# Optimization experiments

Hardware: AMD Instinct MI355X
Metric: run time of the kernel (lower is better)

The kernel has to match this reference:

```python
import jax, jax.numpy as jnp
import numpy as np

N = 10000        # num nodes
E = 640000       # num edges
FIN = 128        # input feature dim
NH = 8           # num heads
FOUT = 16        # out features per head (NH*FOUT == FIN)
NEG_SLOPE = 0.2
EPS = 1e-16


def setup_inputs() -> dict:
    key = jax.random.key(0)
    ks = jax.random.split(key, 7)
    x = jax.random.normal(ks[0], (N, FIN), dtype=jnp.float32)
    edges = jax.random.randint(ks[1], (2, E), 0, N, dtype=jnp.int64)
    # kaiming-uniform-ish init scale
    s = float(np.sqrt(6.0 / FIN))
    W_proj = jax.random.uniform(ks[2], (NH * FOUT, FIN), minval=-s, maxval=s, dtype=jnp.float32)
    W_skip = jax.random.uniform(ks[3], (NH * FOUT, FIN), minval=-s, maxval=s, dtype=jnp.float32)
    sf = float(np.sqrt(6.0 / FOUT))
    score_src = jax.random.uniform(ks[4], (1, NH, FOUT), minval=-sf, maxval=sf, dtype=jnp.float32)
    score_tgt = jax.random.uniform(ks[5], (1, NH, FOUT), minval=-sf, maxval=sf, dtype=jnp.float32)
    bias = jnp.zeros((NH * FOUT,), dtype=jnp.float32)
    return {"x": x, "edges": edges, "W_proj": W_proj, "W_skip": W_skip,
            "score_src": score_src, "score_tgt": score_tgt, "bias": bias}


def reference(x, edges, W_proj, W_skip, score_src, score_tgt, bias):
    src, tgt = edges[0], edges[1]
    # project: [N, NH, FOUT]
    proj = (x @ W_proj.T).reshape(N, NH, FOUT)
    # per-node scores: [N, NH]
    s_src = (proj * score_src).sum(-1)
    s_tgt = (proj * score_tgt).sum(-1)
    # lift to edges and score: [E, NH]
    scores = jax.nn.leaky_relu(s_src[src] + s_tgt[tgt], negative_slope=NEG_SLOPE)
    # neighborhood-aware softmax (global max subtraction, as in original)
    exp_scores = jnp.exp(scores - jnp.max(scores))
    denom = jax.ops.segment_sum(exp_scores, tgt, num_segments=N)  # [N, NH]
    att = exp_scores / (denom[tgt] + EPS)                          # [E, NH]
    # weighted aggregation: [N, NH, FOUT]
    weighted = proj[src] * att[:, :, None]
    out = jax.ops.segment_sum(weighted, tgt, num_segments=N)
    # skip connection (dims differ per-head, so skip_proj is used), concat, bias
    out = out + (x @ W_skip.T).reshape(N, NH, FOUT)
    out = out.reshape(N, NH * FOUT) + bias
    return out
```

## Files before the change

### kernel.cpp

```cpp
#include <hip/hip_runtime.h>
#include <hip/hip_bf16.h>

#define FIN   128
#define NH    8
#define NEG   0.2f
#define HB    128
#define NMAX  10240

typedef __attribute__((ext_vector_type(8))) short short8;
typedef __attribute__((ext_vector_type(4))) float f32x4;

__device__ __forceinline__ short f2bf(float f) {
    unsigned u = __float_as_uint(f);
    return (short)((u + 0x7FFFu + ((u >> 16) & 1u)) >> 16);
}
__device__ __forceinline__ float bflo(unsigned p) { return __uint_as_float(p << 16); }
__device__ __forceinline__ float bfhi(unsigned p) { return __uint_as_float(p & 0xFFFF0000u); }
__device__ __forceinline__ float ld_f(const void* p, int i, bool bf16) {
    if (bf16) {
        unsigned h = ((const unsigned short*)p)[i];
        return __uint_as_float(h << 16);
    }
    return ((const float*)p)[i];
}
__device__ __forceinline__ short8 ld_frag(const void* p, size_t off, bool bf16) {
    if (bf16) return *(const short8*)((const short*)p + off);
    const float* f = (const float*)p + off;
    f32x4 f0 = *(const f32x4*)f;
    f32x4 f1 = *(const f32x4*)(f + 4);
    short8 r;
    r[0] = f2bf(f0[0]); r[1] = f2bf(f0[1]); r[2] = f2bf(f0[2]); r[3] = f2bf(f0[3]);
    r[4] = f2bf(f1[0]); r[5] = f2bf(f1[1]); r[6] = f2bf(f1[2]); r[7] = f2bf(f1[3]);
    return r;
}
__device__ __forceinline__ float escore(float ss, float st) {
    float v = ss + st;
    v = v > 0.f ? v : NEG * v;
    return __expf(fminf(v, 60.f));
}
__device__ __forceinline__ bool wave_bf16(const unsigned* x32) {
    unsigned w  = x32[threadIdx.x & 63];
    unsigned ex = (w >> 7) & 0xFFu;
    return __popcll(__ballot(ex >= 118u && ex <= 130u)) >= 48;
}
__device__ __forceinline__ bool wave_e64(const int* e32) {
    return __popcll(__ballot(e32[2 * (threadIdx.x & 63) + 1] == 0)) == 64;
}

__global__ __launch_bounds__(256) void k_projhist(
    const void* __restrict__ x, const void* __restrict__ Wp,
    const void* __restrict__ Ws,
    const void* __restrict__ ssrcw, const void* __restrict__ stgtw,
    unsigned short* __restrict__ projb, unsigned short* __restrict__ skipb,
    float* __restrict__ s_src, float* __restrict__ s_tgt,
    const int* __restrict__ e32, int* __restrict__ hist2d,
    int N, int E, int tiles, int halfTiles, int projBlocks, int perB)
{
    __shared__ unsigned l32[NMAX / 2];
    if ((int)blockIdx.x >= projBlocks) {
        const bool e64 = wave_e64(e32);
        const int hb = (int)blockIdx.x - projBlocks;
        const int t = threadIdx.x;
        const int nw = (N + 1) >> 1;
        for (int j = t; j < nw; j += 256) l32[j] = 0;
        __syncthreads();
        const int lo = hb * perB;
        const int hi = min(lo + perB, E);
        for (int i = lo + t; i < hi; i += 256) {
            int tg = e64 ? e32[2 * ((size_t)E + i)] : e32[(size_t)E + i];
            atomicAdd(&l32[tg >> 1], 1u << ((tg & 1) << 4));
        }
        __syncthreads();
        for (int j = t; j < N; j += 256)
            hist2d[(size_t)hb * N + j] = (l32[j >> 1] >> ((j & 1) << 4)) & 0xFFFFu;
        return;
    }
    const bool bf16 = wave_bf16((const unsigned*)x);
    const int lane = threadIdx.x & 63;
    const int wt = blockIdx.x * 4 + (threadIdx.x >> 6);
    if (wt >= tiles) return;
    const int mat = (wt >= halfTiles) ? 1 : 0;
    const int m0 = (mat ? wt - halfTiles : wt) * 16;
    const int mr = lane & 15;
    const int kb = lane >> 4;

    short8 a[4];
    const size_t xoff = (size_t)(m0 + mr) * FIN + kb * 8;
#pragma unroll
    for (int s = 0; s < 4; ++s) a[s] = ld_frag(x, xoff + s * 32, bf16);

    const void* W = mat ? Ws : Wp;
    f32x4 acc[8];
#pragma unroll
    for (int c = 0; c < 8; ++c) {
        acc[c] = (f32x4){0.f, 0.f, 0.f, 0.f};
        const size_t woff = (size_t)(c * 16 + mr) * FIN + kb * 8;
#pragma unroll
        for (int s = 0; s < 4; ++s) {
            short8 b = ld_frag(W, woff + s * 32, bf16);
            acc[c] = __builtin_amdgcn_mfma_f32_16x16x32_bf16(a[s], b, acc[c], 0, 0, 0);
        }
    }
    if (mat == 0) {
#pragma unroll
        for (int c = 0; c < 8; ++c) {
            float sw = ld_f(ssrcw, c * 16 + mr, bf16);
            float tw = ld_f(stgtw, c * 16 + mr, bf16);
#pragma unroll
            for (int r = 0; r < 4; ++r) {
                int row = m0 + kb * 4 + r;
                float v = acc[c][r];
                projb[(size_t)row * FIN + c * 16 + mr] = (unsigned short)f2bf(v);
                float vs = v * sw, vt = v * tw;
#pragma unroll
                for (int o = 8; o >= 1; o >>= 1) {
                    vs += __shfl_xor(vs, o);
                    vt += __shfl_xor(vt, o);
                }
                if (mr == 0) {
                    s_src[row * NH + c] = vs;
                    s_tgt[row * NH + c] = vt;
                }
            }
        }
    } else {
#pragma unroll
        for (int c = 0; c < 8; ++c)
#pragma unroll
            for (int r = 0; r < 4; ++r)
                skipb[(size_t)(m0 + kb * 4 + r) * FIN + c * 16 + mr] =
                    (unsigned short)f2bf(acc[c][r]);
    }
}

__global__ __launch_bounds__(256) void k_colscan(
    const int* __restrict__ hist2d, int* __restrict__ pbase,
    int* __restrict__ cnt, int N)
{
    int j = blockIdx.x * 256 + threadIdx.x;
    if (j >= N) return;
    int s = 0;
#pragma unroll 4
    for (int b = 0; b < HB; ++b) {
        int v = hist2d[(size_t)b * N + j];
        pbase[(size_t)b * N + j] = s;
        s += v;
    }
    cnt[j] = s;
}

__global__ __launch_bounds__(256) void k_offscan(const int* __restrict__ cnt,
                                                 int* __restrict__ offs, int N)
{
    const int t = threadIdx.x;
    const int PER = (N + 255) / 256;
    const int base = t * PER;
    int local[40];
    int sum = 0;
    for (int i = 0; i < PER && i < 40; ++i) {
        int idx = base + i;
        int v = (idx < N) ? cnt[idx] : 0;
        local[i] = sum;
        sum += v;
    }
    __shared__ int sd[256];
    sd[t] = sum;
    __syncthreads();
#pragma unroll
    for (int off = 1; off < 256; off <<= 1) {
        int add = (t >= off) ? sd[t - off] : 0;
        __syncthreads();
        sd[t] += add;
        __syncthreads();
    }
    int excl = sd[t] - sum;
    for (int i = 0; i < PER && i < 40; ++i) {
        int idx = base + i;
        if (idx < N) offs[idx] = excl + local[i];
    }
    if (t == 255) offs[N] = sd[255];
}

__global__ __launch_bounds__(256) void k_place(
    const int* __restrict__ e32, const int* __restrict__ offs,
    const int* __restrict__ pbase, int* __restrict__ sorted_src,
    int N, int E, int perB)
{
    __shared__ int cur[NMAX];
    const bool e64 = wave_e64(e32);
    const int b = blockIdx.x, t = threadIdx.x;
    for (int j = t; j < N; j += 256)
        cur[j] = offs[j] + pbase[(size_t)b * N + j];
    __syncthreads();
    const int lo = b * perB;
    const int hi = min(lo + perB, E);
    for (int i = lo + t; i < hi; i += 256) {
        int s, tg;
        if (e64) { s = e32[2 * (size_t)i]; tg = e32[2 * ((size_t)E + i)]; }
        else     { s = e32[i];             tg = e32[(size_t)E + i]; }
        int pos = atomicAdd(&cur[tg], 1);
        sorted_src[pos] = s;
    }
}

__global__ __launch_bounds__(64) void k_aggregate(
    const int* __restrict__ offs, const int* __restrict__ sorted_src,
    const float* __restrict__ s_src, const float* __restrict__ s_tgt,
    const unsigned short* __restrict__ projb, const unsigned short* __restrict__ skipb,
    const void* __restrict__ bias, void* __restrict__ out,
    const unsigned* __restrict__ x32)
{
    const bool bf16 = wave_bf16(x32);
    const int n = blockIdx.x, l = threadIdx.x;
    const int start = offs[n], end = offs[n + 1];
    const int h = l >> 3;
    const int c2 = l * 2;
    const float st = s_tgt[(size_t)n * NH + h];

    float ae0 = 0.f, ao0 = 0.f, ae1 = 0.f, ao1 = 0.f;
    float ae2 = 0.f, ao2 = 0.f, ae3 = 0.f, ao3 = 0.f;
    float d0 = 0.f, d1 = 0.f, d2 = 0.f, d3 = 0.f;
    int e = start;
    for (; e + 4 <= end; e += 4) {
        int s0 = sorted_src[e],     s1 = sorted_src[e + 1];
        int s2 = sorted_src[e + 2], s3 = sorted_src[e + 3];
        float w0 = escore(s_src[(size_t)s0 * NH + h], st);
        float w1 = escore(s_src[(size_t)s1 * NH + h], st);
        float w2 = escore(s_src[(size_t)s2 * NH + h], st);
        float w3 = escore(s_src[(size_t)s3 * NH + h], st);
        unsigned p0 = *(const unsigned*)(projb + (size_t)s0 * FIN + c2);
        unsigned p1 = *(const unsigned*)(projb + (size_t)s1 * FIN + c2);
        unsigned p2 = *(const unsigned*)(projb + (size_t)s2 * FIN + c2);
        unsigned p3 = *(const unsigned*)(projb + (size_t)s3 * FIN + c2);
        ae0 += w0 * bflo(p0); ao0 += w0 * bfhi(p0); d0 += w0;
        ae1 += w1 * bflo(p1); ao1 += w1 * bfhi(p1); d1 += w1;
        ae2 += w2 * bflo(p2); ao2 += w2 * bfhi(p2); d2 += w2;
        ae3 += w3 * bflo(p3); ao3 += w3 * bfhi(p3); d3 += w3;
    }
    for (; e < end; ++e) {
        int s = sorted_src[e];
        float w = escore(s_src[(size_t)s * NH + h], st);
        unsigned p = *(const unsigned*)(projb + (size_t)s * FIN + c2);
        ae0 += w * bflo(p); ao0 += w * bfhi(p); d0 += w;
    }

    float inv = 1.f / (((d0 + d1) + (d2 + d3)) + 1e-16f);
    unsigned skp = *(const unsigned*)(skipb + (size_t)n * FIN + c2);
    float be, bo;
    if (bf16) {
        unsigned bb = *(const unsigned*)((const unsigned short*)bias + c2);
        be = bflo(bb); bo = bfhi(bb);
    } else {
        float2 b2 = *(const float2*)((const float*)bias + c2);
        be = b2.x; bo = b2.y;
    }
    float oe = ((ae0 + ae1) + (ae2 + ae3)) * inv + bflo(skp) + be;
    float oo = ((ao0 + ao1) + (ao2 + ao3)) * inv + bfhi(skp) + bo;
    if (bf16) {
        unsigned pr = ((unsigned)(unsigned short)f2bf(oo) << 16)
                    | (unsigned)(unsigned short)f2bf(oe);
        ((unsigned*)out)[((size_t)n * FIN + c2) >> 1] = pr;
    } else {
        float2 o2; o2.x = oe; o2.y = oo;
        *(float2*)((float*)out + (size_t)n * FIN + c2) = o2;
    }
}

extern "C" void kernel_launch(void* const* d_in, const int* in_sizes, int n_in,
                              void* d_out, int out_size, void* d_ws, size_t ws_size,
                              hipStream_t stream)
{
    const void* x    = d_in[0];
    const int* edges = (const int*)d_in[1];
    const void* Wp   = d_in[2];
    const void* Ws   = d_in[3];
    const void* ssw  = d_in[4];
    const void* stw  = d_in[5];
    const void* bias = d_in[6];

    const int N = in_sizes[0] / FIN;
    const int E = in_sizes[1] / 2;

    unsigned short* projb = (unsigned short*)d_ws;
    unsigned short* skipb = projb + (size_t)N * FIN;
    float* s_src    = (float*)(skipb + (size_t)N * FIN);
    float* s_tgt    = s_src + (size_t)N * NH;
    int* sorted_src = (int*)(s_tgt + (size_t)N * NH);
    int* offs       = sorted_src + E;
    int* cnt        = offs + (N + 1);
    int* hist2d     = cnt + N;
    int* pbase      = hist2d + (size_t)HB * N;

    const int halfTiles  = (N + 15) / 16;
    const int tiles      = 2 * halfTiles;
    const int projBlocks = (tiles + 3) / 4;
    const int perB       = (E + HB - 1) / HB;

    k_projhist<<<projBlocks + HB, 256, 0, stream>>>(
        x, Wp, Ws, ssw, stw, projb, skipb, s_src, s_tgt,
        edges, hist2d, N, E, tiles, halfTiles, projBlocks, perB);
    k_colscan<<<(N + 255) / 256, 256, 0, stream>>>(hist2d, pbase, cnt, N);
    k_offscan<<<1, 256, 0, stream>>>(cnt, offs, N);
    k_place<<<HB, 256, 0, stream>>>(edges, offs, pbase, sorted_src, N, E, perB);
    k_aggregate<<<N, 64, 0, stream>>>(offs, sorted_src, s_src, s_tgt, projb,
                                      skipb, bias, d_out, (const unsigned*)x);
}
```

Measured before the change: 165.9 us.

## Fuse GAT pipeline into one cooperative persistent kernel with grid syncs

Replaces the five separate launches (projection+histogram, column scan, offset scan, placement, aggregation) with a single cooperative kernel of 960 blocks that separates phases with grid.sync. The offset scan becomes a two-level block scan spread over multiple blocks, and aggregation becomes a persistent wave loop over nodes. The aim is to remove launch gaps and the single-block offset scan, at the cost of grid-wide barriers, 40KB shared memory per block limiting occupancy, and less parallelism in the aggregation phase. If the cooperative launch fails, it falls back to the original multi-kernel path.

```diff
diff --git a/kernel.cpp b/kernel.cpp
--- a/kernel.cpp
+++ b/kernel.cpp
@@ -1,11 +1,17 @@
 #include <hip/hip_runtime.h>
 #include <hip/hip_bf16.h>
+#include <hip/hip_cooperative_groups.h>
+
+namespace cg = cooperative_groups;
 
 #define FIN   128
 #define NH    8
 #define NEG   0.2f
 #define HB    128
 #define NMAX  10240
+#define GW0   512
+#define GRID  960
+#define TPB   256
 
 typedef __attribute__((ext_vector_type(8))) short short8;
 typedef __attribute__((ext_vector_type(4))) float f32x4;
@@ -47,38 +53,13 @@
     return __popcll(__ballot(e32[2 * (threadIdx.x & 63) + 1] == 0)) == 64;
 }
 
-__global__ __launch_bounds__(256) void k_projhist(
-    const void* __restrict__ x, const void* __restrict__ Wp,
-    const void* __restrict__ Ws,
-    const void* __restrict__ ssrcw, const void* __restrict__ stgtw,
-    unsigned short* __restrict__ projb, unsigned short* __restrict__ skipb,
-    float* __restrict__ s_src, float* __restrict__ s_tgt,
-    const int* __restrict__ e32, int* __restrict__ hist2d,
-    int N, int E, int tiles, int halfTiles, int projBlocks, int perB)
-{
-    __shared__ unsigned l32[NMAX / 2];
-    if ((int)blockIdx.x >= projBlocks) {
-        const bool e64 = wave_e64(e32);
-        const int hb = (int)blockIdx.x - projBlocks;
-        const int t = threadIdx.x;
-        const int nw = (N + 1) >> 1;
-        for (int j = t; j < nw; j += 256) l32[j] = 0;
-        __syncthreads();
-        const int lo = hb * perB;
-        const int hi = min(lo + perB, E);
-        for (int i = lo + t; i < hi; i += 256) {
-            int tg = e64 ? e32[2 * ((size_t)E + i)] : e32[(size_t)E + i];
-            atomicAdd(&l32[tg >> 1], 1u << ((tg & 1) << 4));
-        }
-        __syncthreads();
-        for (int j = t; j < N; j += 256)
-            hist2d[(size_t)hb * N + j] = (l32[j >> 1] >> ((j & 1) << 4)) & 0xFFFFu;
-        return;
-    }
+__device__ __forceinline__ void gemm_tile(
+    int wt, int halfTiles, const void* x, const void* Wp, const void* Ws,
+    const void* ssrcw, const void* stgtw,
+    unsigned short* projb, unsigned short* skipb, float* s_src, float* s_tgt)
+{
     const bool bf16 = wave_bf16((const unsigned*)x);
     const int lane = threadIdx.x & 63;
-    const int wt = blockIdx.x * 4 + (threadIdx.x >> 6);
-    if (wt >= tiles) return;
     const int mat = (wt >= halfTiles) ? 1 : 0;
     const int m0 = (mat ? wt - halfTiles : wt) * 16;
     const int mr = lane & 15;
@@ -133,85 +114,13 @@
     }
 }
 
-__global__ __launch_bounds__(256) void k_colscan(
-    const int* __restrict__ hist2d, int* __restrict__ pbase,
-    int* __restrict__ cnt, int N)
-{
-    int j = blockIdx.x * 256 + threadIdx.x;
-    if (j >= N) return;
-    int s = 0;
-#pragma unroll 4
-    for (int b = 0; b < HB; ++b) {
-        int v = hist2d[(size_t)b * N + j];
-        pbase[(size_t)b * N + j] = s;
-        s += v;
-    }
-    cnt[j] = s;
-}
-
-__global__ __launch_bounds__(256) void k_offscan(const int* __restrict__ cnt,
-                                                 int* __restrict__ offs, int N)
-{
-    const int t = threadIdx.x;
-    const int PER = (N + 255) / 256;
-    const int base = t * PER;
-    int local[40];
-    int sum = 0;
-    for (int i = 0; i < PER && i < 40; ++i) {
-        int idx = base + i;
-        int v = (idx < N) ? cnt[idx] : 0;
-        local[i] = sum;
-        sum += v;
-    }
-    __shared__ int sd[256];
-    sd[t] = sum;
-    __syncthreads();
-#pragma unroll
-    for (int off = 1; off < 256; off <<= 1) {
-        int add = (t >= off) ? sd[t - off] : 0;
-        __syncthreads();
-        sd[t] += add;
-        __syncthreads();
-    }
-    int excl = sd[t] - sum;
-    for (int i = 0; i < PER && i < 40; ++i) {
-        int idx = base + i;
-        if (idx < N) offs[idx] = excl + local[i];
-    }
-    if (t == 255) offs[N] = sd[255];
-}
-
-__global__ __launch_bounds__(256) void k_place(
-    const int* __restrict__ e32, const int* __restrict__ offs,
-    const int* __restrict__ pbase, int* __restrict__ sorted_src,
-    int N, int E, int perB)
-{
-    __shared__ int cur[NMAX];
-    const bool e64 = wave_e64(e32);
-    const int b = blockIdx.x, t = threadIdx.x;
-    for (int j = t; j < N; j += 256)
-        cur[j] = offs[j] + pbase[(size_t)b * N + j];
-    __syncthreads();
-    const int lo = b * perB;
-    const int hi = min(lo + perB, E);
-    for (int i = lo + t; i < hi; i += 256) {
-        int s, tg;
-        if (e64) { s = e32[2 * (size_t)i]; tg = e32[2 * ((size_t)E + i)]; }
-        else     { s = e32[i];             tg = e32[(size_t)E + i]; }
-        int pos = atomicAdd(&cur[tg], 1);
-        sorted_src[pos] = s;
-    }
-}
-
-__global__ __launch_bounds__(64) void k_aggregate(
-    const int* __restrict__ offs, const int* __restrict__ sorted_src,
-    const float* __restrict__ s_src, const float* __restrict__ s_tgt,
-    const unsigned short* __restrict__ projb, const unsigned short* __restrict__ skipb,
-    const void* __restrict__ bias, void* __restrict__ out,
-    const unsigned* __restrict__ x32)
-{
-    const bool bf16 = wave_bf16(x32);
-    const int n = blockIdx.x, l = threadIdx.x;
+__device__ __forceinline__ void agg_node(
+    int n, bool bf16, const int* offs, const int* sorted_src,
+    const float* s_src, const float* s_tgt,
+    const unsigned short* projb, const unsigned short* skipb,
+    const void* bias, void* out)
+{
+    const int l = threadIdx.x & 63;
     const int start = offs[n], end = offs[n + 1];
     const int h = l >> 3;
     const int c2 = l * 2;
@@ -266,6 +175,220 @@
     }
 }
 
+__global__ __launch_bounds__(TPB, 4) void k_gat(
+    const void* __restrict__ x, const void* __restrict__ Wp,
+    const void* __restrict__ Ws, const void* __restrict__ ssrcw,
+    const void* __restrict__ stgtw, const void* __restrict__ bias,
+    const int* __restrict__ e32, void* __restrict__ out,
+    unsigned short* __restrict__ projb, unsigned short* __restrict__ skipb,
+    float* __restrict__ s_src, float* __restrict__ s_tgt,
+    int* __restrict__ sorted_src, int* __restrict__ offs,
+    int* __restrict__ tmp_off, int* __restrict__ bt,
+    int* __restrict__ hist2d, int* __restrict__ pbase,
+    int N, int E, int perB, int tiles, int halfTiles)
+{
+    cg::grid_group grid = cg::this_grid();
+    __shared__ int sh[NMAX];
+    const int b = blockIdx.x, t = threadIdx.x;
+    const int wv = b * 4 + (t >> 6);
+
+    if (b < HB) {
+        const bool e64 = wave_e64(e32);
+        unsigned* l32 = (unsigned*)sh;
+        const int nw = (N + 1) >> 1;
+        for (int j = t; j < nw; j += TPB) l32[j] = 0;
+        __syncthreads();
+        const int lo = b * perB, hi = min(lo + perB, E);
+        for (int i = lo + t; i < hi; i += TPB) {
+            int tg = e64 ? e32[2 * ((size_t)E + i)] : e32[(size_t)E + i];
+            atomicAdd(&l32[tg >> 1], 1u << ((tg & 1) << 4));
+        }
+        __syncthreads();
+        for (int j = t; j < N; j += TPB)
+            hist2d[(size_t)b * N + j] = (l32[j >> 1] >> ((j & 1) << 4)) & 0xFFFFu;
+    } else {
+        const int wt = wv - GW0;
+        if (wt >= 0 && wt < tiles)
+            gemm_tile(wt, halfTiles, x, Wp, Ws, ssrcw, stgtw,
+                      projb, skipb, s_src, s_tgt);
+    }
+    grid.sync();
+
+    const int CB = (N + TPB - 1) / TPB;
+    if (b < CB) {
+        const int j = b * TPB + t;
+        int s = 0;
+        if (j < N) {
+            for (int r = 0; r < HB; ++r) {
+                int v = hist2d[(size_t)r * N + j];
+                pbase[(size_t)r * N + j] = s;
+                s += v;
+            }
+        }
+        sh[t] = s;
+        __syncthreads();
+#pragma unroll
+        for (int off = 1; off < TPB; off <<= 1) {
+            int add = (t >= off) ? sh[t - off] : 0;
+            __syncthreads();
+            sh[t] += add;
+            __syncthreads();
+        }
+        int incl = sh[t];
+        if (j < N) tmp_off[j] = incl - s;
+        if (t == TPB - 1) bt[b] = incl;
+    }
+    grid.sync();
+
+    if (b < CB) {
+        int carry = 0;
+        for (int r = 0; r < b; ++r) carry += bt[r];
+        const int j = b * TPB + t;
+        if (j < N) offs[j] = tmp_off[j] + carry;
+        if (b == CB - 1 && t == 0) offs[N] = carry + bt[b];
+    }
+    grid.sync();
+
+    if (b < HB) {
+        const bool e64 = wave_e64(e32);
+        for (int j = t; j < N; j += TPB)
+            sh[j] = offs[j] + pbase[(size_t)b * N + j];
+        __syncthreads();
+        const int lo = b * perB, hi = min(lo + perB, E);
+        for (int i = lo + t; i < hi; i += TPB) {
+            int s, tg;
+            if (e64) { s = e32[2 * (size_t)i]; tg = e32[2 * ((size_t)E + i)]; }
+            else     { s = e32[i];             tg = e32[(size_t)E + i]; }
+            int pos = atomicAdd(&sh[tg], 1);
+            sorted_src[pos] = s;
+        }
+    }
+    grid.sync();
+
+    {
+        const bool bf16 = wave_bf16((const unsigned*)x);
+        const int TOTW = (int)gridDim.x * 4;
+        for (int n = wv; n < N; n += TOTW)
+            agg_node(n, bf16, offs, sorted_src, s_src, s_tgt,
+                     projb, skipb, bias, out);
+    }
+}
+
+__global__ __launch_bounds__(256) void k_projhist(
+    const void* __restrict__ x, const void* __restrict__ Wp,
+    const void* __restrict__ Ws,
+    const void* __restrict__ ssrcw, const void* __restrict__ stgtw,
+    unsigned short* __restrict__ projb, unsigned short* __restrict__ skipb,
+    float* __restrict__ s_src, float* __restrict__ s_tgt,
+    const int* __restrict__ e32, int* __restrict__ hist2d,
+    int N, int E, int tiles, int halfTiles, int projBlocks, int perB)
+{
+    __shared__ unsigned l32[NMAX / 2];
+    if ((int)blockIdx.x >= projBlocks) {
+        const bool e64 = wave_e64(e32);
+        const int hb = (int)blockIdx.x - projBlocks;
+        const int t = threadIdx.x;
+        const int nw = (N + 1) >> 1;
+        for (int j = t; j < nw; j += 256) l32[j] = 0;
+        __syncthreads();
+        const int lo = hb * perB;
+        const int hi = min(lo + perB, E);
+        for (int i = lo + t; i < hi; i += 256) {
+            int tg = e64 ? e32[2 * ((size_t)E + i)] : e32[(size_t)E + i];
+            atomicAdd(&l32[tg >> 1], 1u << ((tg & 1) << 4));
+        }
+        __syncthreads();
+        for (int j = t; j < N; j += 256)
+            hist2d[(size_t)hb * N + j] = (l32[j >> 1] >> ((j & 1) << 4)) & 0xFFFFu;
+        return;
+    }
+    const int wt = blockIdx.x * 4 + (threadIdx.x >> 6);
+    if (wt >= tiles) return;
+    gemm_tile(wt, halfTiles, x, Wp, Ws, ssrcw, stgtw, projb, skipb, s_src, s_tgt);
+}
+
+__global__ __launch_bounds__(256) void k_colscan(
+    const int* __restrict__ hist2d, int* __restrict__ pbase,
+    int* __restrict__ cnt, int N)
+{
+    int j = blockIdx.x * 256 + threadIdx.x;
+    if (j >= N) return;
+    int s = 0;
+#pragma unroll 4
+    for (int b = 0; b < HB; ++b) {
+        int v = hist2d[(size_t)b * N + j];
+        pbase[(size_t)b * N + j] = s;
+        s += v;
+    }
+    cnt[j] = s;
+}
+
+__global__ __launch_bounds__(256) void k_offscan(const int* __restrict__ cnt,
+                                                 int* __restrict__ offs, int N)
+{
+    const int t = threadIdx.x;
+    const int PER = (N + 255) / 256;
+    const int base = t * PER;
+    int local[40];
+    int sum = 0;
+    for (int i = 0; i < PER && i < 40; ++i) {
+        int idx = base + i;
+        int v = (idx < N) ? cnt[idx] : 0;
+        local[i] = sum;
+        sum += v;
+    }
+    __shared__ int sd[256];
+    sd[t] = sum;
+    __syncthreads();
+#pragma unroll
+    for (int off = 1; off < 256; off <<= 1) {
+        int add = (t >= off) ? sd[t - off] : 0;
+        __syncthreads();
+        sd[t] += add;
+        __syncthreads();
+    }
+    int excl = sd[t] - sum;
+    for (int i = 0; i < PER && i < 40; ++i) {
+        int idx = base + i;
+        if (idx < N) offs[idx] = excl + local[i];
+    }
+    if (t == 255) offs[N] = sd[255];
+}
+
+__global__ __launch_bounds__(256) void k_place(
+    const int* __restrict__ e32, const int* __restrict__ offs,
+    const int* __restrict__ pbase, int* __restrict__ sorted_src,
+    int N, int E, int perB)
+{
+    __shared__ int cur[NMAX];
+    const bool e64 = wave_e64(e32);
+    const int b = blockIdx.x, t = threadIdx.x;
+    for (int j = t; j < N; j += 256)
+        cur[j] = offs[j] + pbase[(size_t)b * N + j];
+    __syncthreads();
+    const int lo = b * perB;
+    const int hi = min(lo + perB, E);
+    for (int i = lo + t; i < hi; i += 256) {
+        int s, tg;
+        if (e64) { s = e32[2 * (size_t)i]; tg = e32[2 * ((size_t)E + i)]; }
+        else     { s = e32[i];             tg = e32[(size_t)E + i]; }
+        int pos = atomicAdd(&cur[tg], 1);
+        sorted_src[pos] = s;
+    }
+}
+
+__global__ __launch_bounds__(64) void k_aggregate(
+    const int* __restrict__ offs, const int* __restrict__ sorted_src,
+    const float* __restrict__ s_src, const float* __restrict__ s_tgt,
+    const unsigned short* __restrict__ projb, const unsigned short* __restrict__ skipb,
+    const void* __restrict__ bias, void* __restrict__ out,
+    const unsigned* __restrict__ x32)
+{
+    const bool bf16 = wave_bf16(x32);
+    agg_node(blockIdx.x, bf16, offs, sorted_src, s_src, s_tgt,
+             projb, skipb, bias, out);
+}
+
 extern "C" void kernel_launch(void* const* d_in, const int* in_sizes, int n_in,
                               void* d_out, int out_size, void* d_ws, size_t ws_size,
                               hipStream_t stream)
@@ -277,9 +400,10 @@
     const void* ssw  = d_in[4];
     const void* stw  = d_in[5];
     const void* bias = d_in[6];
-
-    const int N = in_sizes[0] / FIN;
-    const int E = in_sizes[1] / 2;
+    void* out        = d_out;
+
+    int N = in_sizes[0] / FIN;
+    int E = in_sizes[1] / 2;
 
     unsigned short* projb = (unsigned short*)d_ws;
     unsigned short* skipb = projb + (size_t)N * FIN;
@@ -287,21 +411,35 @@
     float* s_tgt    = s_src + (size_t)N * NH;
     int* sorted_src = (int*)(s_tgt + (size_t)N * NH);
     int* offs       = sorted_src + E;
-    int* cnt        = offs + (N + 1);
+    int* tmp_off    = offs + (N + 1);
+    int* bt         = tmp_off + N;
+    int* cnt        = bt + 64;
     int* hist2d     = cnt + N;
     int* pbase      = hist2d + (size_t)HB * N;
 
-    const int halfTiles  = (N + 15) / 16;
-    const int tiles      = 2 * halfTiles;
-    const int projBlocks = (tiles + 3) / 4;
-    const int perB       = (E + HB - 1) / HB;
-
-    k_projhist<<<projBlocks + HB, 256, 0, stream>>>(
-        x, Wp, Ws, ssw, stw, projb, skipb, s_src, s_tgt,
-        edges, hist2d, N, E, tiles, halfTiles, projBlocks, perB);
-    k_colscan<<<(N + 255) / 256, 256, 0, stream>>>(hist2d, pbase, cnt, N);
-    k_offscan<<<1, 256, 0, stream>>>(cnt, offs, N);
-    k_place<<<HB, 256, 0, stream>>>(edges, offs, pbase, sorted_src, N, E, perB);
-    k_aggregate<<<N, 64, 0, stream>>>(offs, sorted_src, s_src, s_tgt, projb,
-                                      skipb, bias, d_out, (const unsigned*)x);
-}
+    int halfTiles  = (N + 15) / 16;
+    int tiles      = 2 * halfTiles;
+    int perB       = (E + HB - 1) / HB;
+
+    void* args[] = { (void*)&x, (void*)&Wp, (void*)&Ws, (void*)&ssw, (void*)&stw,
+                     (void*)&bias, (void*)&edges, (void*)&out,
+                     (void*)&projb, (void*)&skipb, (void*)&s_src, (void*)&s_tgt,
+                     (void*)&sorted_src, (void*)&offs, (void*)&tmp_off, (void*)&bt,
+                     (void*)&hist2d, (void*)&pbase,
+                     (void*)&N, (void*)&E, (void*)&perB, (void*)&tiles, (void*)&halfTiles };
+
+    hipError_t err = hipLaunchCooperativeKernel(
+        (const void*)k_gat, dim3(GRID), dim3(TPB), args, 0, stream);
+
+    if (err != hipSuccess) {
+        const int projBlocks = (tiles + 3) / 4;
+        k_projhist<<<projBlocks + HB, 256, 0, stream>>>(
+            x, Wp, Ws, ssw, stw, projb, skipb, s_src, s_tgt,
+            edges, hist2d, N, E, tiles, halfTiles, projBlocks, perB);
+        k_colscan<<<(N + 255) / 256, 256, 0, stream>>>(hist2d, pbase, cnt, N);
+        k_offscan<<<1, 256, 0, stream>>>(cnt, offs, N);
+        k_place<<<HB, 256, 0, stream>>>(edges, offs, pbase, sorted_src, N, E, perB);
+        k_aggregate<<<N, 64, 0, stream>>>(offs, sorted_src, s_src, s_tgt, projb,
+                                          skipb, bias, out, (const unsigned*)x);
+    }
+}
```

After: 598.8 us. 3.61x slower.

## Fuse offset scan into placement kernel and prefetch source indices in aggregation

Applied to the files above, without the earlier changes.

The single-block exclusive scan over per-node counts moves into k_place: every placement block recomputes the scan redundantly, builds its cursor table directly, and block 0 writes the offsets array. This removes one kernel launch and the global round trip for offsets, in exchange for 128 blocks each repeating the scan work. Separately, the aggregation loop now software-pipelines the sorted_src index loads one group of four ahead, so the dependent gathers of scores and projections can issue sooner.

```diff
diff --git a/kernel.cpp b/kernel.cpp
--- a/kernel.cpp
+++ b/kernel.cpp
@@ -149,10 +149,16 @@
     cnt[j] = s;
 }
 
-__global__ __launch_bounds__(256) void k_offscan(const int* __restrict__ cnt,
-                                                 int* __restrict__ offs, int N)
-{
-    const int t = threadIdx.x;
+__global__ __launch_bounds__(256) void k_place(
+    const int* __restrict__ e32, const int* __restrict__ cnt,
+    const int* __restrict__ pbase, int* __restrict__ offs,
+    int* __restrict__ sorted_src, int N, int E, int perB)
+{
+    __shared__ int cur[NMAX];
+    __shared__ int sd[256];
+    const bool e64 = wave_e64(e32);
+    const int b = blockIdx.x, t = threadIdx.x;
+
     const int PER = (N + 255) / 256;
     const int base = t * PER;
     int local[40];
@@ -163,7 +169,6 @@
         local[i] = sum;
         sum += v;
     }
-    __shared__ int sd[256];
     sd[t] = sum;
     __syncthreads();
 #pragma unroll
@@ -173,25 +178,18 @@
         sd[t] += add;
         __syncthreads();
     }
-    int excl = sd[t] - sum;
+    const int excl = sd[t] - sum;
     for (int i = 0; i < PER && i < 40; ++i) {
         int idx = base + i;
-        if (idx < N) offs[idx] = excl + local[i];
-    }
-    if (t == 255) offs[N] = sd[255];
-}
-
-__global__ __launch_bounds__(256) void k_place(
-    const int* __restrict__ e32, const int* __restrict__ offs,
-    const int* __restrict__ pbase, int* __restrict__ sorted_src,
-    int N, int E, int perB)
-{
-    __shared__ int cur[NMAX];
-    const bool e64 = wave_e64(e32);
-    const int b = blockIdx.x, t = threadIdx.x;
-    for (int j = t; j < N; j += 256)
-        cur[j] = offs[j] + pbase[(size_t)b * N + j];
+        if (idx < N) {
+            int o = excl + local[i];
+            cur[idx] = o + pbase[(size_t)b * N + idx];
+            if (b == 0) offs[idx] = o;
+        }
+    }
+    if (b == 0 && t == 255) offs[N] = sd[255];
     __syncthreads();
+
     const int lo = b * perB;
     const int hi = min(lo + perB, E);
     for (int i = lo + t; i < hi; i += 256) {
@@ -220,22 +218,32 @@
     float ae0 = 0.f, ao0 = 0.f, ae1 = 0.f, ao1 = 0.f;
     float ae2 = 0.f, ao2 = 0.f, ae3 = 0.f, ao3 = 0.f;
     float d0 = 0.f, d1 = 0.f, d2 = 0.f, d3 = 0.f;
+
+    const int cnt4 = (end - start) >> 2;
     int e = start;
-    for (; e + 4 <= end; e += 4) {
+    if (cnt4 > 0) {
         int s0 = sorted_src[e],     s1 = sorted_src[e + 1];
         int s2 = sorted_src[e + 2], s3 = sorted_src[e + 3];
-        float w0 = escore(s_src[(size_t)s0 * NH + h], st);
-        float w1 = escore(s_src[(size_t)s1 * NH + h], st);
-        float w2 = escore(s_src[(size_t)s2 * NH + h], st);
-        float w3 = escore(s_src[(size_t)s3 * NH + h], st);
-        unsigned p0 = *(const unsigned*)(projb + (size_t)s0 * FIN + c2);
-        unsigned p1 = *(const unsigned*)(projb + (size_t)s1 * FIN + c2);
-        unsigned p2 = *(const unsigned*)(projb + (size_t)s2 * FIN + c2);
-        unsigned p3 = *(const unsigned*)(projb + (size_t)s3 * FIN + c2);
-        ae0 += w0 * bflo(p0); ao0 += w0 * bfhi(p0); d0 += w0;
-        ae1 += w1 * bflo(p1); ao1 += w1 * bfhi(p1); d1 += w1;
-        ae2 += w2 * bflo(p2); ao2 += w2 * bfhi(p2); d2 += w2;
-        ae3 += w3 * bflo(p3); ao3 += w3 * bfhi(p3); d3 += w3;
+        for (int g = 0; g < cnt4; ++g) {
+            const int t0 = s0, t1 = s1, t2 = s2, t3 = s3;
+            e += 4;
+            if (g + 1 < cnt4) {
+                s0 = sorted_src[e];     s1 = sorted_src[e + 1];
+                s2 = sorted_src[e + 2]; s3 = sorted_src[e + 3];
+            }
+            float w0 = escore(s_src[(size_t)t0 * NH + h], st);
+            float w1 = escore(s_src[(size_t)t1 * NH + h], st);
+            float w2 = escore(s_src[(size_t)t2 * NH + h], st);
+            float w3 = escore(s_src[(size_t)t3 * NH + h], st);
+            unsigned p0 = *(const unsigned*)(projb + (size_t)t0 * FIN + c2);
+            unsigned p1 = *(const unsigned*)(projb + (size_t)t1 * FIN + c2);
+            unsigned p2 = *(const unsigned*)(projb + (size_t)t2 * FIN + c2);
+            unsigned p3 = *(const unsigned*)(projb + (size_t)t3 * FIN + c2);
+            ae0 += w0 * bflo(p0); ao0 += w0 * bfhi(p0); d0 += w0;
+            ae1 += w1 * bflo(p1); ao1 += w1 * bfhi(p1); d1 += w1;
+            ae2 += w2 * bflo(p2); ao2 += w2 * bfhi(p2); d2 += w2;
+            ae3 += w3 * bflo(p3); ao3 += w3 * bfhi(p3); d3 += w3;
+        }
     }
     for (; e < end; ++e) {
         int s = sorted_src[e];
@@ -300,8 +308,7 @@
         x, Wp, Ws, ssw, stw, projb, skipb, s_src, s_tgt,
         edges, hist2d, N, E, tiles, halfTiles, projBlocks, perB);
     k_colscan<<<(N + 255) / 256, 256, 0, stream>>>(hist2d, pbase, cnt, N);
-    k_offscan<<<1, 256, 0, stream>>>(cnt, offs, N);
-    k_place<<<HB, 256, 0, stream>>>(edges, offs, pbase, sorted_src, N, E, perB);
+    k_place<<<HB, 256, 0, stream>>>(edges, cnt, pbase, offs, sorted_src, N, E, perB);
     k_aggregate<<<N, 64, 0, stream>>>(offs, sorted_src, s_src, s_tgt, projb,
                                       skipb, bias, d_out, (const unsigned*)x);
 }
```

After: 165.9 us. No clear change (+0.0%).
